# Kernel optimization log

Measured on AMD Instinct MI355X. Metric: run time of the kernel, lower is better.

## Reference

```python
import jax, jax.numpy as jnp
import numpy as np

VOCAB = 65
N_EMBED = 384
BLOCK = 256
N_HEAD = 6
HEAD_SIZE = 4  # forward uses sa_heads = MultiHeadAttention(4), NOT the Block stack
B, T = 128, 256


def setup_inputs() -> dict:
    key = jax.random.key(0)
    ks = jax.random.split(key, 16)
    s = lambda *sh: 0.02
    inp = {
        "idx": jax.random.randint(ks[0], (B, T), 0, VOCAB),
        "targets": jax.random.randint(ks[1], (B, T), 0, VOCAB),
        "tok_emb": jax.random.normal(ks[2], (VOCAB, N_EMBED), jnp.float32) * 0.02,
        "pos_emb": jax.random.normal(ks[3], (BLOCK, N_EMBED), jnp.float32) * 0.02,
        "Wq": jax.random.normal(ks[4], (N_HEAD, N_EMBED, HEAD_SIZE), jnp.float32) * 0.05,
        "Wk": jax.random.normal(ks[5], (N_HEAD, N_EMBED, HEAD_SIZE), jnp.float32) * 0.05,
        "Wv": jax.random.normal(ks[6], (N_HEAD, N_EMBED, HEAD_SIZE), jnp.float32) * 0.05,
        "Wproj": jax.random.normal(ks[7], (N_HEAD * HEAD_SIZE, N_EMBED), jnp.float32) * 0.05,
        "bproj": jnp.zeros((N_EMBED,), jnp.float32),
        "W1": jax.random.normal(ks[8], (N_EMBED, 4 * N_EMBED), jnp.float32) * 0.02,
        "b1": jnp.zeros((4 * N_EMBED,), jnp.float32),
        "W2": jax.random.normal(ks[9], (4 * N_EMBED, N_EMBED), jnp.float32) * 0.02,
        "b2": jnp.zeros((N_EMBED,), jnp.float32),
        "Wlm": jax.random.normal(ks[10], (N_EMBED, VOCAB), jnp.float32) * 0.02,
        "blm": jnp.zeros((VOCAB,), jnp.float32),
    }
    return inp


def _forward(idx, targets, tok_emb, pos_emb, Wq, Wk, Wv, Wproj, bproj, W1, b1, W2, b2, Wlm, blm):
    Bb, Tt = idx.shape
    x = tok_emb[idx] + pos_emb[:Tt]  # [B,T,C]
    # multi-head attention (manual, causal). NOTE: source scales by n_embed**-0.5 (C of input), not head_size.
    q = jnp.einsum("btc,hcd->bhtd", x, Wq)
    k = jnp.einsum("btc,hcd->bhtd", x, Wk)
    v = jnp.einsum("btc,hcd->bhtd", x, Wv)
    scores = jnp.einsum("bhtd,bhsd->bhts", q, k) * (N_EMBED ** -0.5)
    causal = jnp.tril(jnp.ones((Tt, Tt), bool))
    scores = jnp.where(causal, scores, -jnp.inf)
    w = jax.nn.softmax(scores, axis=-1)  # dropout = identity in eval
    attn = jnp.einsum("bhts,bhsd->bhtd", w, v)
    attn = attn.transpose(0, 2, 1, 3).reshape(Bb, Tt, N_HEAD * HEAD_SIZE)
    x = attn @ Wproj + bproj
    # feed-forward
    x = jax.nn.relu(x @ W1 + b1) @ W2 + b2
    logits = x @ Wlm + blm  # [B,T,V]
    logits_flat = logits.reshape(Bb * Tt, VOCAB)
    t_flat = targets.reshape(Bb * Tt)
    logp = jax.nn.log_softmax(logits_flat, axis=-1)
    loss = -jnp.mean(jnp.take_along_axis(logp, t_flat[:, None], axis=1))
    return logits_flat, loss


def reference(idx, targets, tok_emb, pos_emb, Wq, Wk, Wv, Wproj, bproj, W1, b1, W2, b2, Wlm, blm):
    return _forward(idx, targets, tok_emb, pos_emb, Wq, Wk, Wv, Wproj, bproj, W1, b1, W2, b2, Wlm, blm)
```

## Files before the change

kernel.cpp:

```cpp
#include <hip/hip_runtime.h>
#include <hip/hip_bf16.h>
#include <math.h>

typedef __hip_bfloat16 bf16;
typedef __attribute__((ext_vector_type(8))) short bf16x8;
typedef __attribute__((ext_vector_type(4))) float f32x4;
typedef __attribute__((ext_vector_type(8))) int i32x8;
typedef __attribute__((ext_vector_type(4))) int i32x4;
typedef unsigned char u8;
typedef unsigned int u32;

#define T_SEQ   256
#define C_EMB   384
#define NH      6
#define HS      4
#define NB      128
#define NTOK    (NB * T_SEQ)
#define VOC     65
#define FFDIM   1536
#define QKVW    72
#define PROJK   32
#define XROWS   (VOC * T_SEQ)

#define X2_SCALE    128.0f
#define W1_SCALE    128.0f
#define FF1_DESCALE (1.0f / (128.0f * 128.0f))
#define H1_SCALE    512.0f
#define W2_SCALE    128.0f
#define FF2_DESCALE (1.0f / (512.0f * 128.0f))

__device__ __forceinline__ float bf2f(bf16 x) { return __bfloat162float(x); }
__device__ __forceinline__ bf16  f2b(float x) { return __float2bfloat16(x); }
__device__ __forceinline__ short f2s(float x) { bf16 b = __float2bfloat16(x); return *reinterpret_cast<short*>(&b); }
__device__ __forceinline__ u8 f2fp8(float x) {
    return (u8)(__builtin_amdgcn_cvt_pk_fp8_f32(x, x, 0, false) & 0xff);
}
__device__ __forceinline__ u32 pk4fp8(const float* w) {
    int p = __builtin_amdgcn_cvt_pk_fp8_f32(w[0], w[1], 0, false);
    p = __builtin_amdgcn_cvt_pk_fp8_f32(w[2], w[3], p, true);
    return (u32)p;
}

__device__ __forceinline__ void glds16(const void* g, void* l) {
    __builtin_amdgcn_global_load_lds((const __attribute__((address_space(1))) void*)g,
                                     (__attribute__((address_space(3))) void*)l, 16, 0, 0);
}

__global__ void pack_all_kernel(const float* __restrict__ Wq, const float* __restrict__ Wk,
                                const float* __restrict__ Wv, const float* __restrict__ Wlm,
                                const float* __restrict__ Wproj,
                                const float* __restrict__ W1, const float* __restrict__ W2,
                                const float* __restrict__ tok_emb, const float* __restrict__ pos_emb,
                                bf16* __restrict__ WqkvT, bf16* __restrict__ WlmT,
                                bf16* __restrict__ WprojT, u8* __restrict__ W1f8,
                                u8* __restrict__ W2f8, bf16* __restrict__ xtab,
                                float* __restrict__ lossbuf) {
    int blk = blockIdx.x;
    if (blk == 0 && threadIdx.x == 0) { lossbuf[0] = 0.f; ((int*)lossbuf)[1] = 0; }
    if (blk < 128) {
        int n = blk;
        for (int c = threadIdx.x; c < C_EMB; c += 256) {
            float v = 0.f;
            if (n < QKVW) {
                int sel = n / 24, r = n % 24, h = r >> 2, d = r & 3;
                const float* W = (sel == 0) ? Wq : (sel == 1) ? Wk : Wv;
                v = W[(h * C_EMB + c) * HS + d];
            }
            WqkvT[(size_t)n * C_EMB + c] = f2b(v);
        }
    } else if (blk < 256) {
        int n = blk - 128;
        for (int c = threadIdx.x; c < C_EMB; c += 256)
            WlmT[(size_t)n * C_EMB + c] = f2b(n < VOC ? Wlm[(size_t)c * VOC + n] : 0.f);
    } else if (blk < 640) {
        int n = blk - 256;
        int k = threadIdx.x;
        if (k < PROJK)
            WprojT[(size_t)n * PROJK + k] = f2b(k < 24 ? Wproj[(size_t)k * C_EMB + n] : 0.f);
    } else if (blk < 640 + FFDIM) {
        int n = blk - 640;
        for (int k = threadIdx.x; k < C_EMB; k += 256)
            W1f8[(size_t)n * C_EMB + k] = f2fp8(W1[(size_t)k * FFDIM + n] * W1_SCALE);
    } else if (blk < 640 + FFDIM + C_EMB) {
        int n = blk - 640 - FFDIM;
        for (int k = threadIdx.x; k < FFDIM; k += 256)
            W2f8[(size_t)n * FFDIM + k] = f2fp8(W2[(size_t)k * C_EMB + n] * W2_SCALE);
    } else {
        int base = (blk - (640 + FFDIM + C_EMB)) * 4;
        for (int r = 0; r < 4; ++r) {
            int row = base + r;
            int id = row >> 8, t = row & 255;
            const float* te = tok_emb + (size_t)id * C_EMB;
            const float* pe = pos_emb + (size_t)t * C_EMB;
            bf16* dst = xtab + (size_t)row * C_EMB;
            for (int c = threadIdx.x; c < C_EMB; c += 256)
                dst[c] = f2b(te[c] + pe[c]);
        }
    }
}

__global__ __launch_bounds__(512)
void qkv_gather_kernel(const int* __restrict__ idx, const bf16* __restrict__ xtab,
                       const bf16* __restrict__ Bt, float* __restrict__ outf) {
    __shared__ __align__(16) u8 As[16384];
    __shared__ __align__(16) u8 Bs[16384];
    __shared__ int rowid[128];
    int tid = threadIdx.x, lane = tid & 63, wave = tid >> 6;
    int bm = blockIdx.x * 128;
    int wm = (wave & 1) * 64, wn = (wave >> 1) * 32;
    int lrow = lane & 15, kq = lane >> 4;
    if (tid < 128) { int token = bm + tid; rowid[tid] = idx[token] * T_SEQ + (token & (T_SEQ - 1)); }
    __syncthreads();

    int r0 = tid >> 3;
    int s0 = (((tid & 7) * 16) - (r0 & 7) * 16) & 127;
    int c1 = tid + 512;
    int r1 = c1 >> 3;
    int s1 = (((c1 & 7) * 16) - (r1 & 7) * 16) & 127;
    const u8* xb = (const u8*)xtab;
    const u8* bb = (const u8*)Bt;
    long gA0 = (long)rowid[r0] * 768 + s0;
    long gA1 = (long)rowid[r1] * 768 + s1;
    long gB0 = (long)r0 * 768 + s0;
    long gB1 = (long)r1 * 768 + s1;
    int ro = (lrow & 7) * 16;

    f32x4 acc[4][2] = {};
    for (int k0 = 0; k0 < 768; k0 += 128) {
        glds16(xb + gA0 + k0, As + (size_t)tid * 16);
        glds16(xb + gA1 + k0, As + (size_t)c1 * 16);
        glds16(bb + gB0 + k0, Bs + (size_t)tid * 16);
        glds16(bb + gB1 + k0, Bs + (size_t)c1 * 16);
        __syncthreads();
        #pragma unroll
        for (int ks = 0; ks < 2; ++ks) {
            int off = (ks * 64 + kq * 16 + ro) & 127;
            bf16x8 af[4], bff[2];
            #pragma unroll
            for (int i = 0; i < 4; ++i)
                af[i] = *(const bf16x8*)&As[(size_t)(wm + i * 16 + lrow) * 128 + off];
            #pragma unroll
            for (int i = 0; i < 2; ++i)
                bff[i] = *(const bf16x8*)&Bs[(size_t)(wn + i * 16 + lrow) * 128 + off];
            #pragma unroll
            for (int mi = 0; mi < 4; ++mi)
                #pragma unroll
                for (int ni = 0; ni < 2; ++ni)
                    acc[mi][ni] = __builtin_amdgcn_mfma_f32_16x16x32_bf16(af[mi], bff[ni], acc[mi][ni], 0, 0, 0);
        }
        __syncthreads();
    }

    #pragma unroll
    for (int ni = 0; ni < 2; ++ni) {
        int col = wn + ni * 16 + lrow;
        if (col >= QKVW) continue;
        #pragma unroll
        for (int mi = 0; mi < 4; ++mi) {
            int orow = bm + wm + mi * 16 + kq * 4;
            #pragma unroll
            for (int r = 0; r < 4; ++r)
                outf[(size_t)(orow + r) * QKVW + col] = acc[mi][ni][r];
        }
    }
}

__global__ void attn_kernel(const float* __restrict__ qkv,
                            bf16* __restrict__ attnT) {
    int bh = blockIdx.x;
    int b = bh / NH, h = bh % NH;
    int t = threadIdx.x;
    __shared__ float4 kv[T_SEQ][2];
    const float* base = qkv + (size_t)(b * T_SEQ) * QKVW;
    kv[t][0] = *(const float4*)(base + t * QKVW + 24 + h * HS);
    kv[t][1] = *(const float4*)(base + t * QKVW + 48 + h * HS);
    __syncthreads();
    const float scale = 0.05103103630798288f;
    float4 q = *(const float4*)(base + t * QKVW + h * HS);
    float qx = q.x * scale, qy = q.y * scale, qz = q.z * scale, qw = q.w * scale;
    float sum0 = 0.f, sum1 = 0.f;
    float o0x = 0.f, o0y = 0.f, o0z = 0.f, o0w = 0.f;
    float o1x = 0.f, o1y = 0.f, o1z = 0.f, o1w = 0.f;
    int s = 0;
    for (; s + 1 <= t; s += 2) {
        float4 k0 = kv[s][0],     v0 = kv[s][1];
        float4 k1 = kv[s + 1][0], v1 = kv[s + 1][1];
        float p0 = __expf(qx * k0.x + qy * k0.y + qz * k0.z + qw * k0.w);
        float p1 = __expf(qx * k1.x + qy * k1.y + qz * k1.z + qw * k1.w);
        sum0 += p0; sum1 += p1;
        o0x += p0 * v0.x; o0y += p0 * v0.y; o0z += p0 * v0.z; o0w += p0 * v0.w;
        o1x += p1 * v1.x; o1y += p1 * v1.y; o1z += p1 * v1.z; o1w += p1 * v1.w;
    }
    if (s <= t) {
        float4 k0 = kv[s][0], v0 = kv[s][1];
        float p0 = __expf(qx * k0.x + qy * k0.y + qz * k0.z + qw * k0.w);
        sum0 += p0;
        o0x += p0 * v0.x; o0y += p0 * v0.y; o0z += p0 * v0.z; o0w += p0 * v0.w;
    }
    float inv = 1.f / (sum0 + sum1);
    bf16* out = attnT + (size_t)(b * T_SEQ + t) * PROJK + h * HS;
    out[0] = f2b((o0x + o1x) * inv);
    out[1] = f2b((o0y + o1y) * inv);
    out[2] = f2b((o0z + o1z) * inv);
    out[3] = f2b((o0w + o1w) * inv);
    if (h == 0) {
        bf16* pad = attnT + (size_t)(b * T_SEQ + t) * PROJK + 24;
        *(uint4*)pad = uint4{0, 0, 0, 0};
    }
}

__global__ __launch_bounds__(512, 2)
void ff_mega_kernel(const bf16* __restrict__ attnT, const bf16* __restrict__ WprojT,
                    const float* __restrict__ bproj,
                    const u8* __restrict__ W1f8, const float* __restrict__ b1,
                    const u8* __restrict__ W2f8, const float* __restrict__ b2,
                    bf16* __restrict__ x3) {
    __shared__ __align__(16) u8 smem[147456];
    u8* x2_lds = smem;
    u8* bs1    = smem + 49152;
    u8* h1t    = smem + 81920;
    u8* bs2    = smem + 98304;
    short* As_p = (short*)(smem + 49152);
    short* Bs_p = (short*)(smem + 57344);

    int tid  = threadIdx.x;
    int lane = tid & 63;
    int wave = tid >> 6;
    int bm   = blockIdx.x * 128;
    int wm   = (wave & 1) * 64;
    int lrow  = lane & 15;
    int khalf = lane >> 4;

    {
        int row = tid >> 2;
        int i0 = (tid & 3) * 16;
        int selem = ((i0 - ((row >> 1) & 3) * 16) & 63) >> 1;
        glds16(attnT + (size_t)(bm + row) * PROJK + selem, As_p + (size_t)tid * 8);
        #pragma unroll
        for (int p = 0; p < 3; ++p) {
            int c = tid + p * 512;
            int rowb = c >> 2;
            int sel2 = (((c & 3) * 16 - ((rowb >> 1) & 3) * 16) & 63) >> 1;
            glds16(WprojT + (size_t)rowb * PROJK + sel2, Bs_p + (size_t)c * 8);
        }
    }
    __syncthreads();

    int wn6 = (wave >> 1) * 96;
    f32x4 accp[4][6] = {};
    {
        int arot16 = ((lrow >> 1) & 3) * 16;
        int roff = ((khalf * 16 + arot16) & 63) >> 1;
        bf16x8 afp[4], bfp[6];
        #pragma unroll
        for (int i = 0; i < 4; ++i)
            afp[i] = *(const bf16x8*)&As_p[(size_t)(wm + i * 16 + lrow) * 32 + roff];
        #pragma unroll
        for (int i = 0; i < 6; ++i)
            bfp[i] = *(const bf16x8*)&Bs_p[(size_t)(wn6 + i * 16 + lrow) * 32 + roff];
        #pragma unroll
        for (int mi = 0; mi < 4; ++mi)
            #pragma unroll
            for (int ni = 0; ni < 6; ++ni)
                accp[mi][ni] = __builtin_amdgcn_mfma_f32_16x16x32_bf16(bfp[ni], afp[mi], accp[mi][ni], 0, 0, 0);
    }
    __syncthreads();

    int r0 = tid >> 3;
    int s0 = (((tid & 7) * 16) - (r0 & 7) * 16) & 127;

    {
        const u8* g = W1f8 + (size_t)r0 * 384 + s0;
        glds16(g, bs1 + (size_t)tid * 16);
        glds16(g + (size_t)64 * 384, bs1 + 8192 + (size_t)tid * 16);
        const u8* g2 = W2f8 + (size_t)r0 * 1536 + s0;
        #pragma unroll
        for (int j = 0; j < 6; ++j)
            glds16(g2 + (size_t)j * 64 * 1536, bs2 + (size_t)j * 8192 + (size_t)tid * 16);
    }

    #pragma unroll
    for (int mi = 0; mi < 4; ++mi) {
        int m = wm + mi * 16 + lrow;
        #pragma unroll
        for (int ni = 0; ni < 6; ++ni) {
            int n0 = wn6 + ni * 16 + khalf * 4;
            float4 bv = *(const float4*)(bproj + n0);
            float w[4];
            w[0] = (accp[mi][ni][0] + bv.x) * X2_SCALE;
            w[1] = (accp[mi][ni][1] + bv.y) * X2_SCALE;
            w[2] = (accp[mi][ni][2] + bv.z) * X2_SCALE;
            w[3] = (accp[mi][ni][3] + bv.w) * X2_SCALE;
            *(u32*)&x2_lds[(size_t)(n0 >> 7) * 16384 + (size_t)m * 128 +
                           (((n0 & 127) + (m & 7) * 16) & 127)] = pk4fp8(w);
        }
    }
    __syncthreads();

    int arot8 = (lrow & 7) * 16;
    int off0 = (khalf * 32 + arot8) & 127;
    int off1 = (off0 + 16) & 127;
    int wn2 = (wave >> 1) * 32;

    f32x4 acc1[4][2] = {};
    f32x4 acc2[4][6] = {};

    for (int nt = 0; nt < 12; ++nt) {
        #pragma unroll
        for (int kk = 0; kk < 3; ++kk) {
            int stp = nt * 3 + kk;
            int cur = stp & 1;
            int nxt = stp + 1;
            if (nxt < 36) {
                int nnt = nxt / 3, nk0 = (nxt % 3) * 128;
                const u8* g = W1f8 + (size_t)(nnt * 128 + r0) * 384 + nk0 + s0;
                u8* dst = bs1 + (size_t)(nxt & 1) * 16384;
                glds16(g, dst + (size_t)tid * 16);
                glds16(g + (size_t)64 * 384, dst + 8192 + (size_t)tid * 16);
            }
            const u8* abase = x2_lds + (size_t)kk * 16384;
            const u8* bbase = bs1 + (size_t)cur * 16384;
            i32x8 a[4], b[2];
            #pragma unroll
            for (int i = 0; i < 4; ++i) {
                const u8* rp = abase + (size_t)(wm + i * 16 + lrow) * 128;
                i32x4 lo = *(const i32x4*)(rp + off0);
                i32x4 hi = *(const i32x4*)(rp + off1);
                a[i][0]=lo[0]; a[i][1]=lo[1]; a[i][2]=lo[2]; a[i][3]=lo[3];
                a[i][4]=hi[0]; a[i][5]=hi[1]; a[i][6]=hi[2]; a[i][7]=hi[3];
            }
            #pragma unroll
            for (int i = 0; i < 2; ++i) {
                const u8* rp = bbase + (size_t)(wn2 + i * 16 + lrow) * 128;
                i32x4 lo = *(const i32x4*)(rp + off0);
                i32x4 hi = *(const i32x4*)(rp + off1);
                b[i][0]=lo[0]; b[i][1]=lo[1]; b[i][2]=lo[2]; b[i][3]=lo[3];
                b[i][4]=hi[0]; b[i][5]=hi[1]; b[i][6]=hi[2]; b[i][7]=hi[3];
            }
            #pragma unroll
            for (int mi = 0; mi < 4; ++mi)
                #pragma unroll
                for (int ni = 0; ni < 2; ++ni)
                    acc1[mi][ni] = __builtin_amdgcn_mfma_scale_f32_16x16x128_f8f6f4(
                        b[ni], a[mi], acc1[mi][ni], 0, 0,
                        0, 0x7f7f7f7f, 0, 0x7f7f7f7f);
            __syncthreads();
        }

        #pragma unroll
        for (int mi = 0; mi < 4; ++mi) {
            int m = wm + mi * 16 + lrow;
            #pragma unroll
            for (int ni = 0; ni < 2; ++ni) {
                int n0 = wn2 + ni * 16 + khalf * 4;
                float4 bv = *(const float4*)(b1 + nt * 128 + n0);
                float w[4];
                w[0] = fmaxf(acc1[mi][ni][0] * FF1_DESCALE + bv.x, 0.f) * H1_SCALE;
                w[1] = fmaxf(acc1[mi][ni][1] * FF1_DESCALE + bv.y, 0.f) * H1_SCALE;
                w[2] = fmaxf(acc1[mi][ni][2] * FF1_DESCALE + bv.z, 0.f) * H1_SCALE;
                w[3] = fmaxf(acc1[mi][ni][3] * FF1_DESCALE + bv.w, 0.f) * H1_SCALE;
                *(u32*)&h1t[(size_t)m * 128 + ((n0 + (m & 7) * 16) & 127)] = pk4fp8(w);
                acc1[mi][ni] = f32x4{0.f, 0.f, 0.f, 0.f};
            }
        }
        __syncthreads();

        {
            i32x8 a2[4];
            #pragma unroll
            for (int i = 0; i < 4; ++i) {
                const u8* rp = h1t + (size_t)(wm + i * 16 + lrow) * 128;
                i32x4 lo = *(const i32x4*)(rp + off0);
                i32x4 hi = *(const i32x4*)(rp + off1);
                a2[i][0]=lo[0]; a2[i][1]=lo[1]; a2[i][2]=lo[2]; a2[i][3]=lo[3];
                a2[i][4]=hi[0]; a2[i][5]=hi[1]; a2[i][6]=hi[2]; a2[i][7]=hi[3];
            }
            #pragma unroll
            for (int half = 0; half < 2; ++half) {
                i32x8 bw[3];
                #pragma unroll
                for (int j = 0; j < 3; ++j) {
                    int ni = half * 3 + j;
                    const u8* rp = bs2 + (size_t)(wn6 + ni * 16 + lrow) * 128;
                    i32x4 lo = *(const i32x4*)(rp + off0);
                    i32x4 hi = *(const i32x4*)(rp + off1);
                    bw[j][0]=lo[0]; bw[j][1]=lo[1]; bw[j][2]=lo[2]; bw[j][3]=lo[3];
                    bw[j][4]=hi[0]; bw[j][5]=hi[1]; bw[j][6]=hi[2]; bw[j][7]=hi[3];
                }
                #pragma unroll
                for (int mi = 0; mi < 4; ++mi)
                    #pragma unroll
                    for (int j = 0; j < 3; ++j)
                        acc2[mi][half * 3 + j] = __builtin_amdgcn_mfma_scale_f32_16x16x128_f8f6f4(
                            bw[j], a2[mi], acc2[mi][half * 3 + j], 0, 0,
                            0, 0x7f7f7f7f, 0, 0x7f7f7f7f);
            }
        }
        __syncthreads();

        if (nt + 1 < 12) {
            const u8* g2 = W2f8 + (size_t)r0 * 1536 + (nt + 1) * 128 + s0;
            #pragma unroll
            for (int j = 0; j < 6; ++j)
                glds16(g2 + (size_t)j * 64 * 1536, bs2 + (size_t)j * 8192 + (size_t)tid * 16);
        }
    }

    u8* Ep = smem;
    #pragma unroll
    for (int mi = 0; mi < 4; ++mi) {
        int m = wm + mi * 16 + lrow;
        #pragma unroll
        for (int ni = 0; ni < 6; ++ni) {
            int n0 = wn6 + ni * 16 + khalf * 4;
            float4 bv = *(const float4*)(b2 + n0);
            union { short s[4]; uint2 u; } pk;
            pk.s[0] = f2s(acc2[mi][ni][0] * FF2_DESCALE + bv.x);
            pk.s[1] = f2s(acc2[mi][ni][1] * FF2_DESCALE + bv.y);
            pk.s[2] = f2s(acc2[mi][ni][2] * FF2_DESCALE + bv.z);
            pk.s[3] = f2s(acc2[mi][ni][3] * FF2_DESCALE + bv.w);
            *(uint2*)&Ep[(size_t)m * 768 + ((n0 >> 7) << 8) +
                         ((((n0 & 127) * 2) + (m & 7) * 16) & 255)] = pk.u;
        }
    }
    __syncthreads();
    #pragma unroll
    for (int p = 0; p < 12; ++p) {
        int c = tid + p * 512;
        int row = c / 48;
        int sl = c - row * 48;
        int g0 = sl * 16;
        int chunk = g0 >> 8;
        int loc = g0 & 255;
        uint4 v = *(const uint4*)&Ep[(size_t)row * 768 + (chunk << 8) +
                                     ((loc + (row & 7) * 16) & 255)];
        *(uint4*)((u8*)x3 + (size_t)(bm + row) * 768 + g0) = v;
    }
}

__global__ __launch_bounds__(512)
void lm_loss_kernel(const bf16* __restrict__ A, const bf16* __restrict__ Bt,
                    const float* __restrict__ bias, const int* __restrict__ targets,
                    float* __restrict__ outf, float* __restrict__ lossbuf,
                    float* __restrict__ out_loss, int M, int K) {
    __shared__ short As[128][32];
    __shared__ short Bs[128][32];
    __shared__ float Ls[128][66];
    __shared__ float red[128];
    int tid  = threadIdx.x;
    int lane = tid & 63;
    int wave = tid >> 6;
    int bm = blockIdx.x * 128;
    int wm = (wave & 1) * 64;
    int wn = (wave >> 1) * 32;
    int lrow  = lane & 15;
    int khalf = lane >> 4;

    int row = tid >> 2;
    int i0 = (tid & 3) * 16;
    int selem = ((i0 - ((row >> 1) & 3) * 16) & 63) >> 1;
    int arot = ((lrow >> 1) & 3) * 16;
    int roff = ((khalf * 16 + arot) & 63) >> 1;

    f32x4 acc[4][2] = {};
    for (int k0 = 0; k0 < K; k0 += 32) {
        glds16(A  + (size_t)(bm + row) * K + k0 + selem, (short*)As + (size_t)tid * 8);
        glds16(Bt + (size_t)row * K + k0 + selem,        (short*)Bs + (size_t)tid * 8);
        __syncthreads();

        bf16x8 af[4], bff[2];
        #pragma unroll
        for (int i = 0; i < 4; ++i)
            af[i] = *(const bf16x8*)&As[wm + i * 16 + lrow][roff];
        #pragma unroll
        for (int i = 0; i < 2; ++i)
            bff[i] = *(const bf16x8*)&Bs[wn + i * 16 + lrow][roff];
        #pragma unroll
        for (int mi = 0; mi < 4; ++mi)
            #pragma unroll
            for (int ni = 0; ni < 2; ++ni)
                acc[mi][ni] = __builtin_amdgcn_mfma_f32_16x16x32_bf16(af[mi], bff[ni], acc[mi][ni], 0, 0, 0);
        __syncthreads();
    }

    #pragma unroll
    for (int ni = 0; ni < 2; ++ni) {
        int col = wn + ni * 16 + lrow;
        if (col >= VOC) continue;
        float bv = bias[col];
        #pragma unroll
        for (int mi = 0; mi < 4; ++mi) {
            int lr = wm + mi * 16 + khalf * 4;
            #pragma unroll
            for (int r = 0; r < 4; ++r) {
                float v = acc[mi][ni][r] + bv;
                outf[(size_t)(bm + lr + r) * VOC + col] = v;
                Ls[lr + r][col] = v;
            }
        }
    }
    __syncthreads();

    if (tid < 128) {
        int token = bm + tid;
        int tgt = targets[token];
        float m = -1e30f, s = 0.f;
        #pragma unroll 8
        for (int c = 0; c < VOC; ++c) {
            float v = Ls[tid][c];
            float mn = fmaxf(m, v);
            s = s * __expf(m - mn) + __expf(v - mn);
            m = mn;
        }
        red[tid] = m + logf(s) - Ls[tid][tgt];
    }
    __syncthreads();
    if (tid < 64) {
        float s = red[tid] + red[tid + 64];
        #pragma unroll
        for (int off = 32; off > 0; off >>= 1) s += __shfl_xor(s, off);
        if (tid == 0) {
            atomicAdd(&lossbuf[0], s);
            __threadfence();
            int done = atomicAdd(&((int*)lossbuf)[1], 1);
            if (done == (NTOK / 128) - 1) {
                __threadfence();
                float total = atomicAdd(&lossbuf[0], 0.0f);
                out_loss[0] = total / (float)NTOK;
            }
        }
    }
}

extern "C" void kernel_launch(void* const* d_in, const int* in_sizes, int n_in,
                              void* d_out, int out_size, void* d_ws, size_t ws_size,
                              hipStream_t stream) {
    const int*   idx     = (const int*)  d_in[0];
    const int*   targets = (const int*)  d_in[1];
    const float* tok_emb = (const float*)d_in[2];
    const float* pos_emb = (const float*)d_in[3];
    const float* Wq      = (const float*)d_in[4];
    const float* Wk      = (const float*)d_in[5];
    const float* Wv      = (const float*)d_in[6];
    const float* Wproj   = (const float*)d_in[7];
    const float* bproj   = (const float*)d_in[8];
    const float* W1      = (const float*)d_in[9];
    const float* b1      = (const float*)d_in[10];
    const float* W2      = (const float*)d_in[11];
    const float* b2      = (const float*)d_in[12];
    const float* Wlm     = (const float*)d_in[13];
    const float* blm     = (const float*)d_in[14];

    char* ws = (char*)d_ws;
    bf16*  WprojT = (bf16*) (ws + 0);
    float* qkvbuf = (float*)(ws + 25165824);
    bf16*  attnT  = (bf16*) (ws + 34603008);
    bf16*  xtab   = (bf16*) (ws + 37748736);
    bf16*  x3     = (bf16*) (ws + 163577856);
    float* lossbuf= (float*)(ws + 188743680);
    u8*    W1f8   = (u8*)   (ws + 188874752);
    u8*    W2f8   = (u8*)   (ws + 190054400);
    bf16*  WqkvT  = (bf16*) (ws + 191234048);
    bf16*  WlmT   = (bf16*) (ws + 191332352);

    float* out_logits = (float*)d_out;
    float* out_loss   = out_logits + (size_t)NTOK * VOC;

    pack_all_kernel<<<640 + FFDIM + C_EMB + XROWS / 4, 256, 0, stream>>>(
        Wq, Wk, Wv, Wlm, Wproj, W1, W2, tok_emb, pos_emb,
        WqkvT, WlmT, WprojT, W1f8, W2f8, xtab, lossbuf);

    qkv_gather_kernel<<<NTOK / 128, 512, 0, stream>>>(idx, xtab, WqkvT, qkvbuf);
    attn_kernel<<<NB * NH, T_SEQ, 0, stream>>>(qkvbuf, attnT);

    ff_mega_kernel<<<NTOK / 128, 512, 0, stream>>>(attnT, WprojT, bproj,
                                                   W1f8, b1, W2f8, b2, x3);

    lm_loss_kernel<<<NTOK / 128, 512, 0, stream>>>(x3, WlmT, blm, targets,
                                                   out_logits, lossbuf, out_loss, NTOK, C_EMB);
}
```

Baseline: 210.0 us.

## Halve FF mega-kernel row tile and read W2 directly from global

The fused proj/FF kernel now handles 64 rows per block instead of 128, with the grid doubled and launch bounds raised to target four blocks per CU. LDS drops from 144KB to 64KB because the W2 shared-memory staging buffer is removed and the W2 fragments are loaded straight from global memory (expected to hit in cache) inside the FF2 loop. The goal is higher occupancy and less LDS pressure. In exchange, each weight tile is reused across fewer rows and the W2 loads are uncoalesced global reads on the critical path.

```diff
diff --git a/kernel.cpp b/kernel.cpp
--- a/kernel.cpp
+++ b/kernel.cpp
@@ -209,57 +209,57 @@
     }
 }
 
-__global__ __launch_bounds__(512, 2)
+__global__ __launch_bounds__(512, 4)
 void ff_mega_kernel(const bf16* __restrict__ attnT, const bf16* __restrict__ WprojT,
                     const float* __restrict__ bproj,
                     const u8* __restrict__ W1f8, const float* __restrict__ b1,
                     const u8* __restrict__ W2f8, const float* __restrict__ b2,
                     bf16* __restrict__ x3) {
-    __shared__ __align__(16) u8 smem[147456];
+    __shared__ __align__(16) u8 smem[65536];
     u8* x2_lds = smem;
-    u8* bs1    = smem + 49152;
-    u8* h1t    = smem + 81920;
-    u8* bs2    = smem + 98304;
-    short* As_p = (short*)(smem + 49152);
-    short* Bs_p = (short*)(smem + 57344);
+    u8* bs1    = smem + 24576;
+    u8* h1t    = smem + 57344;
+    short* As_p = (short*)(smem + 24576);
+    short* Bs_p = (short*)(smem + 28672);
 
     int tid  = threadIdx.x;
     int lane = tid & 63;
     int wave = tid >> 6;
-    int bm   = blockIdx.x * 128;
-    int wm   = (wave & 1) * 64;
+    int bm   = blockIdx.x * 64;
     int lrow  = lane & 15;
     int khalf = lane >> 4;
-
-    {
+    int wmh = (wave & 1) * 32;
+    int wn4 = (wave >> 1) * 96;
+    int wn1 = (wave >> 1) * 32;
+
+    if (tid < 256) {
         int row = tid >> 2;
         int i0 = (tid & 3) * 16;
         int selem = ((i0 - ((row >> 1) & 3) * 16) & 63) >> 1;
         glds16(attnT + (size_t)(bm + row) * PROJK + selem, As_p + (size_t)tid * 8);
-        #pragma unroll
-        for (int p = 0; p < 3; ++p) {
-            int c = tid + p * 512;
-            int rowb = c >> 2;
-            int sel2 = (((c & 3) * 16 - ((rowb >> 1) & 3) * 16) & 63) >> 1;
-            glds16(WprojT + (size_t)rowb * PROJK + sel2, Bs_p + (size_t)c * 8);
-        }
-    }
-    __syncthreads();
-
-    int wn6 = (wave >> 1) * 96;
-    f32x4 accp[4][6] = {};
+    }
+    #pragma unroll
+    for (int p = 0; p < 3; ++p) {
+        int c = tid + p * 512;
+        int rowb = c >> 2;
+        int sel2 = (((c & 3) * 16 - ((rowb >> 1) & 3) * 16) & 63) >> 1;
+        glds16(WprojT + (size_t)rowb * PROJK + sel2, Bs_p + (size_t)c * 8);
+    }
+    __syncthreads();
+
+    f32x4 accp[2][6] = {};
     {
         int arot16 = ((lrow >> 1) & 3) * 16;
         int roff = ((khalf * 16 + arot16) & 63) >> 1;
-        bf16x8 afp[4], bfp[6];
-        #pragma unroll
-        for (int i = 0; i < 4; ++i)
-            afp[i] = *(const bf16x8*)&As_p[(size_t)(wm + i * 16 + lrow) * 32 + roff];
+        bf16x8 afp[2], bfp[6];
+        #pragma unroll
+        for (int i = 0; i < 2; ++i)
+            afp[i] = *(const bf16x8*)&As_p[(size_t)(wmh + i * 16 + lrow) * 32 + roff];
         #pragma unroll
         for (int i = 0; i < 6; ++i)
-            bfp[i] = *(const bf16x8*)&Bs_p[(size_t)(wn6 + i * 16 + lrow) * 32 + roff];
-        #pragma unroll
-        for (int mi = 0; mi < 4; ++mi)
+            bfp[i] = *(const bf16x8*)&Bs_p[(size_t)(wn4 + i * 16 + lrow) * 32 + roff];
+        #pragma unroll
+        for (int mi = 0; mi < 2; ++mi)
             #pragma unroll
             for (int ni = 0; ni < 6; ++ni)
                 accp[mi][ni] = __builtin_amdgcn_mfma_f32_16x16x32_bf16(bfp[ni], afp[mi], accp[mi][ni], 0, 0, 0);
@@ -273,25 +273,21 @@
         const u8* g = W1f8 + (size_t)r0 * 384 + s0;
         glds16(g, bs1 + (size_t)tid * 16);
         glds16(g + (size_t)64 * 384, bs1 + 8192 + (size_t)tid * 16);
-        const u8* g2 = W2f8 + (size_t)r0 * 1536 + s0;
-        #pragma unroll
-        for (int j = 0; j < 6; ++j)
-            glds16(g2 + (size_t)j * 64 * 1536, bs2 + (size_t)j * 8192 + (size_t)tid * 16);
     }
 
     #pragma unroll
-    for (int mi = 0; mi < 4; ++mi) {
-        int m = wm + mi * 16 + lrow;
+    for (int mi = 0; mi < 2; ++mi) {
+        int m = wmh + mi * 16 + lrow;
         #pragma unroll
         for (int ni = 0; ni < 6; ++ni) {
-            int n0 = wn6 + ni * 16 + khalf * 4;
+            int n0 = wn4 + ni * 16 + khalf * 4;
             float4 bv = *(const float4*)(bproj + n0);
             float w[4];
             w[0] = (accp[mi][ni][0] + bv.x) * X2_SCALE;
             w[1] = (accp[mi][ni][1] + bv.y) * X2_SCALE;
             w[2] = (accp[mi][ni][2] + bv.z) * X2_SCALE;
             w[3] = (accp[mi][ni][3] + bv.w) * X2_SCALE;
-            *(u32*)&x2_lds[(size_t)(n0 >> 7) * 16384 + (size_t)m * 128 +
+            *(u32*)&x2_lds[(size_t)(n0 >> 7) * 8192 + (size_t)m * 128 +
                            (((n0 & 127) + (m & 7) * 16) & 127)] = pk4fp8(w);
         }
     }
@@ -300,30 +296,27 @@
     int arot8 = (lrow & 7) * 16;
     int off0 = (khalf * 32 + arot8) & 127;
     int off1 = (off0 + 16) & 127;
-    int wn2 = (wave >> 1) * 32;
-
-    f32x4 acc1[4][2] = {};
-    f32x4 acc2[4][6] = {};
+
+    f32x4 acc1[2][2] = {};
+    f32x4 acc2[2][6] = {};
 
     for (int nt = 0; nt < 12; ++nt) {
         #pragma unroll
         for (int kk = 0; kk < 3; ++kk) {
             int stp = nt * 3 + kk;
-            int cur = stp & 1;
-            int nxt = stp + 1;
-            if (nxt < 36) {
-                int nnt = nxt / 3, nk0 = (nxt % 3) * 128;
+            if (stp + 1 < 36) {
+                int nnt = (stp + 1) / 3, nk0 = ((stp + 1) % 3) * 128;
                 const u8* g = W1f8 + (size_t)(nnt * 128 + r0) * 384 + nk0 + s0;
-                u8* dst = bs1 + (size_t)(nxt & 1) * 16384;
+                u8* dst = bs1 + (size_t)((stp + 1) & 1) * 16384;
                 glds16(g, dst + (size_t)tid * 16);
                 glds16(g + (size_t)64 * 384, dst + 8192 + (size_t)tid * 16);
             }
-            const u8* abase = x2_lds + (size_t)kk * 16384;
-            const u8* bbase = bs1 + (size_t)cur * 16384;
-            i32x8 a[4], b[2];
-            #pragma unroll
-            for (int i = 0; i < 4; ++i) {
-                const u8* rp = abase + (size_t)(wm + i * 16 + lrow) * 128;
+            const u8* abase = x2_lds + (size_t)kk * 8192;
+            const u8* bbase = bs1 + (size_t)(stp & 1) * 16384;
+            i32x8 a[2], b[2];
+            #pragma unroll
+            for (int i = 0; i < 2; ++i) {
+                const u8* rp = abase + (size_t)(wmh + i * 16 + lrow) * 128;
                 i32x4 lo = *(const i32x4*)(rp + off0);
                 i32x4 hi = *(const i32x4*)(rp + off1);
                 a[i][0]=lo[0]; a[i][1]=lo[1]; a[i][2]=lo[2]; a[i][3]=lo[3];
@@ -331,14 +324,14 @@
             }
             #pragma unroll
             for (int i = 0; i < 2; ++i) {
-                const u8* rp = bbase + (size_t)(wn2 + i * 16 + lrow) * 128;
+                const u8* rp = bbase + (size_t)(wn1 + i * 16 + lrow) * 128;
                 i32x4 lo = *(const i32x4*)(rp + off0);
                 i32x4 hi = *(const i32x4*)(rp + off1);
                 b[i][0]=lo[0]; b[i][1]=lo[1]; b[i][2]=lo[2]; b[i][3]=lo[3];
                 b[i][4]=hi[0]; b[i][5]=hi[1]; b[i][6]=hi[2]; b[i][7]=hi[3];
             }
             #pragma unroll
-            for (int mi = 0; mi < 4; ++mi)
+            for (int mi = 0; mi < 2; ++mi)
                 #pragma unroll
                 for (int ni = 0; ni < 2; ++ni)
                     acc1[mi][ni] = __builtin_amdgcn_mfma_scale_f32_16x16x128_f8f6f4(
@@ -348,11 +341,11 @@
         }
 
         #pragma unroll
-        for (int mi = 0; mi < 4; ++mi) {
-            int m = wm + mi * 16 + lrow;
+        for (int mi = 0; mi < 2; ++mi) {
+            int m = wmh + mi * 16 + lrow;
             #pragma unroll
             for (int ni = 0; ni < 2; ++ni) {
-                int n0 = wn2 + ni * 16 + khalf * 4;
+                int n0 = wn1 + ni * 16 + khalf * 4;
                 float4 bv = *(const float4*)(b1 + nt * 128 + n0);
                 float w[4];
                 w[0] = fmaxf(acc1[mi][ni][0] * FF1_DESCALE + bv.x, 0.f) * H1_SCALE;
@@ -366,10 +359,10 @@
         __syncthreads();
 
         {
-            i32x8 a2[4];
-            #pragma unroll
-            for (int i = 0; i < 4; ++i) {
-                const u8* rp = h1t + (size_t)(wm + i * 16 + lrow) * 128;
+            i32x8 a2[2];
+            #pragma unroll
+            for (int i = 0; i < 2; ++i) {
+                const u8* rp = h1t + (size_t)(wmh + i * 16 + lrow) * 128;
                 i32x4 lo = *(const i32x4*)(rp + off0);
                 i32x4 hi = *(const i32x4*)(rp + off1);
                 a2[i][0]=lo[0]; a2[i][1]=lo[1]; a2[i][2]=lo[2]; a2[i][3]=lo[3];
@@ -380,15 +373,15 @@
                 i32x8 bw[3];
                 #pragma unroll
                 for (int j = 0; j < 3; ++j) {
-                    int ni = half * 3 + j;
-                    const u8* rp = bs2 + (size_t)(wn6 + ni * 16 + lrow) * 128;
-                    i32x4 lo = *(const i32x4*)(rp + off0);
-                    i32x4 hi = *(const i32x4*)(rp + off1);
+                    int n = wn4 + (half * 3 + j) * 16 + lrow;
+                    const u8* p = W2f8 + (size_t)n * 1536 + nt * 128 + khalf * 32;
+                    i32x4 lo = *(const i32x4*)p;
+                    i32x4 hi = *(const i32x4*)(p + 16);
                     bw[j][0]=lo[0]; bw[j][1]=lo[1]; bw[j][2]=lo[2]; bw[j][3]=lo[3];
                     bw[j][4]=hi[0]; bw[j][5]=hi[1]; bw[j][6]=hi[2]; bw[j][7]=hi[3];
                 }
                 #pragma unroll
-                for (int mi = 0; mi < 4; ++mi)
+                for (int mi = 0; mi < 2; ++mi)
                     #pragma unroll
                     for (int j = 0; j < 3; ++j)
                         acc2[mi][half * 3 + j] = __builtin_amdgcn_mfma_scale_f32_16x16x128_f8f6f4(
@@ -397,22 +390,15 @@
             }
         }
         __syncthreads();
-
-        if (nt + 1 < 12) {
-            const u8* g2 = W2f8 + (size_t)r0 * 1536 + (nt + 1) * 128 + s0;
-            #pragma unroll
-            for (int j = 0; j < 6; ++j)
-                glds16(g2 + (size_t)j * 64 * 1536, bs2 + (size_t)j * 8192 + (size_t)tid * 16);
-        }
     }
 
     u8* Ep = smem;
     #pragma unroll
-    for (int mi = 0; mi < 4; ++mi) {
-        int m = wm + mi * 16 + lrow;
+    for (int mi = 0; mi < 2; ++mi) {
+        int m = wmh + mi * 16 + lrow;
         #pragma unroll
         for (int ni = 0; ni < 6; ++ni) {
-            int n0 = wn6 + ni * 16 + khalf * 4;
+            int n0 = wn4 + ni * 16 + khalf * 4;
             float4 bv = *(const float4*)(b2 + n0);
             union { short s[4]; uint2 u; } pk;
             pk.s[0] = f2s(acc2[mi][ni][0] * FF2_DESCALE + bv.x);
@@ -425,7 +411,7 @@
     }
     __syncthreads();
     #pragma unroll
-    for (int p = 0; p < 12; ++p) {
+    for (int p = 0; p < 6; ++p) {
         int c = tid + p * 512;
         int row = c / 48;
         int sl = c - row * 48;
@@ -573,8 +559,8 @@
     qkv_gather_kernel<<<NTOK / 128, 512, 0, stream>>>(idx, xtab, WqkvT, qkvbuf);
     attn_kernel<<<NB * NH, T_SEQ, 0, stream>>>(qkvbuf, attnT);
 
-    ff_mega_kernel<<<NTOK / 128, 512, 0, stream>>>(attnT, WprojT, bproj,
-                                                   W1f8, b1, W2f8, b2, x3);
+    ff_mega_kernel<<<NTOK / 64, 512, 0, stream>>>(attnT, WprojT, bproj,
+                                                  W1f8, b1, W2f8, b2, x3);
 
     lm_loss_kernel<<<NTOK / 128, 512, 0, stream>>>(x3, WlmT, blm, targets,
                                                    out_logits, lossbuf, out_loss, NTOK, C_EMB);
```

New measurement: 255.0 us. +21.4%, slower.

## Widen FF1 tile to 256 columns and read W2 fragments directly from global

Applied to the files above, without the earlier changes.

The FF1 N-tile doubles from 128 to 256 hidden units per step, halving the outer loop count and the number of FF1→FF2 barrier phases. Each wave now holds four FF1 accumulators, and the h1 staging buffer grows to 256 bytes per row. The W2 LDS staging buffer is removed, and W2 fp8 fragments are loaded straight from global memory into registers for the FF2 MFMAs. This drops the per-step W2 LDS fill and its synchronisation, but exposes FF2 to global load latency and adds register pressure under the 512-thread, 2-blocks-per-CU launch bounds.

```diff
diff --git a/kernel.cpp b/kernel.cpp
--- a/kernel.cpp
+++ b/kernel.cpp
@@ -218,8 +218,7 @@
     __shared__ __align__(16) u8 smem[147456];
     u8* x2_lds = smem;
     u8* bs1    = smem + 49152;
-    u8* h1t    = smem + 81920;
-    u8* bs2    = smem + 98304;
+    u8* h1t    = smem + 114688;
     short* As_p = (short*)(smem + 49152);
     short* Bs_p = (short*)(smem + 57344);
 
@@ -227,9 +226,11 @@
     int lane = tid & 63;
     int wave = tid >> 6;
     int bm   = blockIdx.x * 128;
-    int wm   = (wave & 1) * 64;
     int lrow  = lane & 15;
     int khalf = lane >> 4;
+    int wm  = (wave & 1) * 64;
+    int wn6 = (wave >> 1) * 96;
+    int wn4 = (wave >> 1) * 64;
 
     {
         int row = tid >> 2;
@@ -246,7 +247,6 @@
     }
     __syncthreads();
 
-    int wn6 = (wave >> 1) * 96;
     f32x4 accp[4][6] = {};
     {
         int arot16 = ((lrow >> 1) & 3) * 16;
@@ -266,17 +266,12 @@
     }
     __syncthreads();
 
-    int r0 = tid >> 3;
-    int s0 = (((tid & 7) * 16) - (r0 & 7) * 16) & 127;
-
-    {
-        const u8* g = W1f8 + (size_t)r0 * 384 + s0;
-        glds16(g, bs1 + (size_t)tid * 16);
-        glds16(g + (size_t)64 * 384, bs1 + 8192 + (size_t)tid * 16);
-        const u8* g2 = W2f8 + (size_t)r0 * 1536 + s0;
-        #pragma unroll
-        for (int j = 0; j < 6; ++j)
-            glds16(g2 + (size_t)j * 64 * 1536, bs2 + (size_t)j * 8192 + (size_t)tid * 16);
+    #pragma unroll
+    for (int p = 0; p < 4; ++p) {
+        int c = tid + p * 512;
+        int row = c >> 3;
+        int sr = (((c & 7) * 16) - (row & 7) * 16) & 127;
+        glds16(W1f8 + (size_t)row * 384 + sr, bs1 + (size_t)c * 16);
     }
 
     #pragma unroll
@@ -300,27 +295,29 @@
     int arot8 = (lrow & 7) * 16;
     int off0 = (khalf * 32 + arot8) & 127;
     int off1 = (off0 + 16) & 127;
-    int wn2 = (wave >> 1) * 32;
-
-    f32x4 acc1[4][2] = {};
+
+    f32x4 acc1[4][4] = {};
     f32x4 acc2[4][6] = {};
 
-    for (int nt = 0; nt < 12; ++nt) {
+    for (int nt = 0; nt < 6; ++nt) {
         #pragma unroll
         for (int kk = 0; kk < 3; ++kk) {
             int stp = nt * 3 + kk;
-            int cur = stp & 1;
-            int nxt = stp + 1;
-            if (nxt < 36) {
-                int nnt = nxt / 3, nk0 = (nxt % 3) * 128;
-                const u8* g = W1f8 + (size_t)(nnt * 128 + r0) * 384 + nk0 + s0;
-                u8* dst = bs1 + (size_t)(nxt & 1) * 16384;
-                glds16(g, dst + (size_t)tid * 16);
-                glds16(g + (size_t)64 * 384, dst + 8192 + (size_t)tid * 16);
+            if (stp + 1 < 18) {
+                int nnt = (stp + 1) / 3, nk0 = ((stp + 1) % 3) * 128;
+                u8* dst = bs1 + (size_t)((stp + 1) & 1) * 32768;
+                #pragma unroll
+                for (int p = 0; p < 4; ++p) {
+                    int c = tid + p * 512;
+                    int row = c >> 3;
+                    int sr = (((c & 7) * 16) - (row & 7) * 16) & 127;
+                    glds16(W1f8 + (size_t)(nnt * 256 + row) * 384 + nk0 + sr,
+                           dst + (size_t)c * 16);
+                }
             }
             const u8* abase = x2_lds + (size_t)kk * 16384;
-            const u8* bbase = bs1 + (size_t)cur * 16384;
-            i32x8 a[4], b[2];
+            const u8* bbase = bs1 + (size_t)(stp & 1) * 32768;
+            i32x8 a[4];
             #pragma unroll
             for (int i = 0; i < 4; ++i) {
                 const u8* rp = abase + (size_t)(wm + i * 16 + lrow) * 128;
@@ -330,20 +327,25 @@
                 a[i][4]=hi[0]; a[i][5]=hi[1]; a[i][6]=hi[2]; a[i][7]=hi[3];
             }
             #pragma unroll
-            for (int i = 0; i < 2; ++i) {
-                const u8* rp = bbase + (size_t)(wn2 + i * 16 + lrow) * 128;
-                i32x4 lo = *(const i32x4*)(rp + off0);
-                i32x4 hi = *(const i32x4*)(rp + off1);
-                b[i][0]=lo[0]; b[i][1]=lo[1]; b[i][2]=lo[2]; b[i][3]=lo[3];
-                b[i][4]=hi[0]; b[i][5]=hi[1]; b[i][6]=hi[2]; b[i][7]=hi[3];
-            }
-            #pragma unroll
-            for (int mi = 0; mi < 4; ++mi)
+            for (int nh = 0; nh < 2; ++nh) {
+                i32x8 b[2];
                 #pragma unroll
-                for (int ni = 0; ni < 2; ++ni)
-                    acc1[mi][ni] = __builtin_amdgcn_mfma_scale_f32_16x16x128_f8f6f4(
-                        b[ni], a[mi], acc1[mi][ni], 0, 0,
-                        0, 0x7f7f7f7f, 0, 0x7f7f7f7f);
+                for (int j = 0; j < 2; ++j) {
+                    int ni = nh * 2 + j;
+                    const u8* rp = bbase + (size_t)(wn4 + ni * 16 + lrow) * 128;
+                    i32x4 lo = *(const i32x4*)(rp + off0);
+                    i32x4 hi = *(const i32x4*)(rp + off1);
+                    b[j][0]=lo[0]; b[j][1]=lo[1]; b[j][2]=lo[2]; b[j][3]=lo[3];
+                    b[j][4]=hi[0]; b[j][5]=hi[1]; b[j][6]=hi[2]; b[j][7]=hi[3];
+                }
+                #pragma unroll
+                for (int mi = 0; mi < 4; ++mi)
+                    #pragma unroll
+                    for (int j = 0; j < 2; ++j)
+                        acc1[mi][nh * 2 + j] = __builtin_amdgcn_mfma_scale_f32_16x16x128_f8f6f4(
+                            b[j], a[mi], acc1[mi][nh * 2 + j], 0, 0,
+                            0, 0x7f7f7f7f, 0, 0x7f7f7f7f);
+            }
             __syncthreads();
         }
 
@@ -351,27 +353,30 @@
         for (int mi = 0; mi < 4; ++mi) {
             int m = wm + mi * 16 + lrow;
             #pragma unroll
-            for (int ni = 0; ni < 2; ++ni) {
-                int n0 = wn2 + ni * 16 + khalf * 4;
-                float4 bv = *(const float4*)(b1 + nt * 128 + n0);
+            for (int ni = 0; ni < 4; ++ni) {
+                int n0 = wn4 + ni * 16 + khalf * 4;
+                float4 bv = *(const float4*)(b1 + nt * 256 + n0);
                 float w[4];
                 w[0] = fmaxf(acc1[mi][ni][0] * FF1_DESCALE + bv.x, 0.f) * H1_SCALE;
                 w[1] = fmaxf(acc1[mi][ni][1] * FF1_DESCALE + bv.y, 0.f) * H1_SCALE;
                 w[2] = fmaxf(acc1[mi][ni][2] * FF1_DESCALE + bv.z, 0.f) * H1_SCALE;
                 w[3] = fmaxf(acc1[mi][ni][3] * FF1_DESCALE + bv.w, 0.f) * H1_SCALE;
-                *(u32*)&h1t[(size_t)m * 128 + ((n0 + (m & 7) * 16) & 127)] = pk4fp8(w);
+                *(u32*)&h1t[(size_t)m * 256 + ((n0 + (m & 7) * 16) & 255)] = pk4fp8(w);
                 acc1[mi][ni] = f32x4{0.f, 0.f, 0.f, 0.f};
             }
         }
         __syncthreads();
 
-        {
+        #pragma unroll
+        for (int sk = 0; sk < 2; ++sk) {
             i32x8 a2[4];
             #pragma unroll
             for (int i = 0; i < 4; ++i) {
-                const u8* rp = h1t + (size_t)(wm + i * 16 + lrow) * 128;
-                i32x4 lo = *(const i32x4*)(rp + off0);
-                i32x4 hi = *(const i32x4*)(rp + off1);
+                const u8* rp = h1t + (size_t)(wm + i * 16 + lrow) * 256;
+                int o0 = (sk * 128 + khalf * 32 + arot8) & 255;
+                int o1 = (sk * 128 + khalf * 32 + 16 + arot8) & 255;
+                i32x4 lo = *(const i32x4*)(rp + o0);
+                i32x4 hi = *(const i32x4*)(rp + o1);
                 a2[i][0]=lo[0]; a2[i][1]=lo[1]; a2[i][2]=lo[2]; a2[i][3]=lo[3];
                 a2[i][4]=hi[0]; a2[i][5]=hi[1]; a2[i][6]=hi[2]; a2[i][7]=hi[3];
             }
@@ -380,10 +385,10 @@
                 i32x8 bw[3];
                 #pragma unroll
                 for (int j = 0; j < 3; ++j) {
-                    int ni = half * 3 + j;
-                    const u8* rp = bs2 + (size_t)(wn6 + ni * 16 + lrow) * 128;
-                    i32x4 lo = *(const i32x4*)(rp + off0);
-                    i32x4 hi = *(const i32x4*)(rp + off1);
+                    int n = wn6 + (half * 3 + j) * 16 + lrow;
+                    const u8* p = W2f8 + (size_t)n * 1536 + nt * 256 + sk * 128 + khalf * 32;
+                    i32x4 lo = *(const i32x4*)p;
+                    i32x4 hi = *(const i32x4*)(p + 16);
                     bw[j][0]=lo[0]; bw[j][1]=lo[1]; bw[j][2]=lo[2]; bw[j][3]=lo[3];
                     bw[j][4]=hi[0]; bw[j][5]=hi[1]; bw[j][6]=hi[2]; bw[j][7]=hi[3];
                 }
@@ -397,13 +402,6 @@
             }
         }
         __syncthreads();
-
-        if (nt + 1 < 12) {
-            const u8* g2 = W2f8 + (size_t)r0 * 1536 + (nt + 1) * 128 + s0;
-            #pragma unroll
-            for (int j = 0; j < 6; ++j)
-                glds16(g2 + (size_t)j * 64 * 1536, bs2 + (size_t)j * 8192 + (size_t)tid * 16);
-        }
     }
 
     u8* Ep = smem;
```

After: 247.2 us. 1.18x slower.
